# Performance work log

Measured on AMD Instinct MI355X. Metric: run time of the kernel, lower is better.

## Reference

```python
import jax, jax.numpy as jnp
import numpy as np

HEADS = 8
HIDDEN = 1536
HEAD_DIM = HIDDEN // HEADS
SCALE = HEAD_DIM ** -0.5


def setup_inputs() -> dict:
    key = jax.random.key(0)
    ks = jax.random.split(key, 10)
    B, S_IMG, S_TXT = 32, 1024, 77
    w = 0.02
    return {
        "img": jax.random.normal(ks[0], (B, S_IMG, HIDDEN), dtype=jnp.float32),
        "text": jax.random.normal(ks[1], (B, S_TXT, HIDDEN), dtype=jnp.float32),
        "Wq": jax.random.normal(ks[2], (HIDDEN, HIDDEN), dtype=jnp.float32) * w,
        "bq": jnp.zeros((HIDDEN,), dtype=jnp.float32),
        "Wk": jax.random.normal(ks[3], (HIDDEN, HIDDEN), dtype=jnp.float32) * w,
        "bk": jnp.zeros((HIDDEN,), dtype=jnp.float32),
        "Wv": jax.random.normal(ks[4], (HIDDEN, HIDDEN), dtype=jnp.float32) * w,
        "bv": jnp.zeros((HIDDEN,), dtype=jnp.float32),
        "Wo": jax.random.normal(ks[5], (HIDDEN, HIDDEN), dtype=jnp.float32) * w,
        "bo": jnp.zeros((HIDDEN,), dtype=jnp.float32),
    }


def reference(img, text, Wq, bq, Wk, bk, Wv, bv, Wo, bo):
    B, Sq, D = img.shape
    Sk = text.shape[1]
    # QKV projections (nn.Linear: y = x @ W.T + b)
    q = img @ Wq.T + bq    # [B, Sq, D]
    k = text @ Wk.T + bk   # [B, Sk, D]
    v = text @ Wv.T + bv
    # detach trick: position 0 of k/v has gradient stopped; forward value unchanged
    k0 = jax.lax.stop_gradient(k[:, :1, :])
    k = jnp.concatenate([k0, k[:, 1:, :]], axis=1)
    v0 = jax.lax.stop_gradient(v[:, :1, :])
    v = jnp.concatenate([v0, v[:, 1:, :]], axis=1)
    # split heads
    q = q.reshape(B, Sq, HEADS, HEAD_DIM)
    k = k.reshape(B, Sk, HEADS, HEAD_DIM)
    v = v.reshape(B, Sk, HEADS, HEAD_DIM)
    # attention scores and probs (mask is None in this module)
    scores = jnp.einsum("bqhd,bkhd->bhqk", q, k) * SCALE  # [B, H, Sq, Sk]
    probs = jax.nn.softmax(scores, axis=-1)
    out = jnp.einsum("bhqk,bkhd->bqhd", probs, v).reshape(B, Sq, D)
    return out @ Wo.T + bo
```

## Files before the change

kernel.cpp:

```cpp
#include <hip/hip_runtime.h>
#include <hip/hip_bf16.h>


typedef unsigned short u16;
typedef _Float16 f16x8 __attribute__((ext_vector_type(8)));
typedef __attribute__((ext_vector_type(8))) short s16x8;
typedef __attribute__((ext_vector_type(4))) float f32x4;
typedef __attribute__((ext_vector_type(4))) short s16x4;

#define MFMAH(a, b, c) __builtin_amdgcn_mfma_f32_16x16x32_f16(a, b, c, 0, 0, 0)

__device__ __forceinline__ u16 f2h(float x) {
    _Float16 h = (_Float16)x;
    return __builtin_bit_cast(u16, h);
}

__device__ __forceinline__ void gload16(const u16* g, const u16* l) {
    __builtin_amdgcn_global_load_lds(
        (const __attribute__((address_space(1))) unsigned int*)g,
        (__attribute__((address_space(3))) unsigned int*)l, 16, 0, 0);
}

__device__ __forceinline__ int rh(int r) { return (r >> 1) & 3; }

__global__ void conv_h(const float* __restrict__ x, u16* __restrict__ h, int n8) {
    const int i = blockIdx.x * 256 + threadIdx.x;
    if (i >= n8) return;
    const f32x4 a = ((const f32x4*)x)[2 * i];
    const f32x4 b = ((const f32x4*)x)[2 * i + 1];
    u16 o[8];
#pragma unroll
    for (int j = 0; j < 4; ++j) { o[j] = f2h(a[j]); o[4 + j] = f2h(b[j]); }
    *(s16x8*)&h[(size_t)i << 3] = *(s16x8*)o;
}

struct Conv5Args {
    const float* x[5];
    u16* h[5];
    int n8[5];
};

__global__ void conv_h5(Conv5Args A) {
    const int z = blockIdx.y;
    const int i = blockIdx.x * 256 + threadIdx.x;
    if (i >= A.n8[z]) return;
    const float* x = A.x[z];
    const f32x4 a = ((const f32x4*)x)[2 * i];
    const f32x4 b = ((const f32x4*)x)[2 * i + 1];
    u16 o[8];
#pragma unroll
    for (int j = 0; j < 4; ++j) { o[j] = f2h(a[j]); o[4 + j] = f2h(b[j]); }
    *(s16x8*)&A.h[z][(size_t)i << 3] = *(s16x8*)o;
}

template <int OUTF32>
__global__ __launch_bounds__(256, 4) void gemm_h_nt(
    const u16* __restrict__ A,
    const u16* __restrict__ B0, const float* __restrict__ bias0, void* __restrict__ C0,
    const u16* __restrict__ B1, const float* __restrict__ bias1, void* __restrict__ C1,
    int M, int N, int K, int nby) {
    __shared__ u16 lds[16384];

    const u16* B = B0; const float* bias = bias0; void* Cout = C0;
    if (blockIdx.z) { B = B1; bias = bias1; Cout = C1; }

    const int nwg = gridDim.x;
    const int q8 = nwg >> 3, r8 = nwg & 7;
    const int xcd = blockIdx.x & 7, loc = blockIdx.x >> 3;
    const int wgid = (xcd < r8 ? xcd * (q8 + 1) : r8 * (q8 + 1) + (xcd - r8) * q8) + loc;
    const int bx = wgid / nby, by = wgid - bx * nby;
    const int row0 = bx * 128, col0 = by * 128;

    const int t = threadIdx.x, lane = t & 63, w = t >> 6;
    const int wm = w >> 1, wn = w & 1;
    const int l15 = lane & 15, lhi = lane >> 4;

    const u16* gpA[2]; const u16* gpB[2];
    int lofA[2], lofB[2];
#pragma unroll
    for (int it = 0; it < 2; ++it) {
        const int ci = it * 256 + t;
        const int row = ci >> 2, slot = ci & 3;
        const int gs = slot ^ rh(row);
        int ar = row0 + row; if (ar > M - 1) ar = M - 1;
        gpA[it] = A + (size_t)ar * K + (gs << 3);
        gpB[it] = B + (size_t)(col0 + row) * K + (gs << 3);
        lofA[it] = ci * 8;
        lofB[it] = 8192 + ci * 8;
    }

    const int ss = rh(l15);
    int aof[4], bof[4];
#pragma unroll
    for (int i = 0; i < 4; ++i) {
        const int ar = wm * 64 + i * 16 + l15;
        aof[i] = ar * 32 + ((lhi ^ ss) << 3);
        const int br = wn * 64 + i * 16 + l15;
        bof[i] = 8192 + br * 32 + ((lhi ^ ss) << 3);
    }

    f32x4 acc[4][4] = {};
    const int NT = K >> 5;

    for (int tt = 0; tt < NT; ++tt) {
        const size_t kk = (size_t)tt << 5;
        if (tt) __syncthreads();
        gload16(gpA[0] + kk, lds + lofA[0]);
        gload16(gpA[1] + kk, lds + lofA[1]);
        gload16(gpB[0] + kk, lds + lofB[0]);
        gload16(gpB[1] + kk, lds + lofB[1]);
        __syncthreads();

        f16x8 a[4];
#pragma unroll
        for (int mf = 0; mf < 4; ++mf) a[mf] = *(const f16x8*)&lds[aof[mf]];
#pragma unroll
        for (int nf = 0; nf < 4; ++nf) {
            const f16x8 b = *(const f16x8*)&lds[bof[nf]];
#pragma unroll
            for (int mf = 0; mf < 4; ++mf)
                acc[mf][nf] = MFMAH(a[mf], b, acc[mf][nf]);
        }
    }

#pragma unroll
    for (int nf = 0; nf < 4; ++nf) {
        const int col = col0 + wn * 64 + nf * 16 + l15;
        const float bs = bias[col];
#pragma unroll
        for (int mf = 0; mf < 4; ++mf) {
            const int row = row0 + wm * 64 + mf * 16 + (lhi << 2);
#pragma unroll
            for (int r = 0; r < 4; ++r) {
                if (row + r < M) {
                    const float v = acc[mf][nf][r] + bs;
                    if (OUTF32) ((float*)Cout)[(size_t)(row + r) * N + col] = v;
                    else        ((u16*)Cout)[(size_t)(row + r) * N + col] = f2h(v);
                }
            }
        }
    }
}

#define ALDK 200
#define ALDP 104

__global__ void attn_fused(const u16* __restrict__ qbuf, const u16* __restrict__ kbuf,
                           const u16* __restrict__ vbuf, u16* __restrict__ obuf) {
    __shared__ u16 Ks[80 * ALDK];
    __shared__ u16 Pls[64 * ALDP];
    __shared__ u16 Vt[96 * ALDP];

    const int t = threadIdx.x, lane = t & 63, w = t >> 6;
    const int qt = blockIdx.x, h = blockIdx.y, b = blockIdx.z;
    const int l15 = lane & 15, lhi = lane >> 4;

    f16x8 qf[6];
    {
        const size_t qrow = (size_t)(b * 1024 + qt * 64 + w * 16 + l15);
        const u16* qp = qbuf + qrow * 1536 + h * 192 + (lhi << 3);
#pragma unroll
        for (int kt = 0; kt < 6; ++kt) qf[kt] = *(const f16x8*)(qp + kt * 32);
    }

    for (int c = t; c < 80 * 24; c += 256) {
        const int s = c / 24, d8 = (c - s * 24) << 3;
        s16x8 val = {};
        if (s < 77) val = *(const s16x8*)&kbuf[(size_t)(b * 77 + s) * 1536 + h * 192 + d8];
        *(s16x8*)&Ks[s * ALDK + d8] = val;
    }
    for (int c = t; c < 96 * 12; c += 256) {
        const int s = c % 96, d8 = (c / 96) << 3;
        s16x8 val = {};
        if (s < 77) val = *(const s16x8*)&vbuf[(size_t)(b * 77 + s) * 1536 + h * 192 + d8];
#pragma unroll
        for (int j = 0; j < 8; ++j) Vt[(d8 + j) * ALDP + s] = (u16)val[j];
    }
    {
        const int row = w * 16 + l15;
        s16x4 z = {0, 0, 0, 0};
        *(s16x4*)&Pls[row * ALDP + 80 + (lhi << 2)] = z;
    }
    __syncthreads();

    f32x4 sacc[5] = {};
#pragma unroll
    for (int kt = 0; kt < 6; ++kt) {
#pragma unroll
        for (int nf = 0; nf < 5; ++nf) {
            f16x8 kf = *(const f16x8*)&Ks[(nf * 16 + l15) * ALDK + kt * 32 + (lhi << 3)];
            sacc[nf] = MFMAH(qf[kt], kf, sacc[nf]);
        }
    }

    float rps[4];
    const float scale = 0.07216878364870323f;
#pragma unroll
    for (int r = 0; r < 4; ++r) {
        float m = -1e30f;
#pragma unroll
        for (int nf = 0; nf < 5; ++nf) {
            const int c = nf * 16 + l15;
            const float sv = sacc[nf][r] * scale;
            if (c < 77) m = fmaxf(m, sv);
        }
#pragma unroll
        for (int off = 1; off < 16; off <<= 1) m = fmaxf(m, __shfl_xor(m, off));
        float sum = 0.f;
#pragma unroll
        for (int nf = 0; nf < 5; ++nf) {
            const int c = nf * 16 + l15;
            const float p = (c < 77) ? __expf(sacc[nf][r] * scale - m) : 0.f;
            sacc[nf][r] = p;
            sum += p;
        }
#pragma unroll
        for (int off = 1; off < 16; off <<= 1) sum += __shfl_xor(sum, off);
        rps[r] = 1.0f / sum;
    }

#pragma unroll
    for (int r = 0; r < 4; ++r)
#pragma unroll
        for (int nf = 0; nf < 5; ++nf)
            Pls[(w * 16 + (lhi << 2) + r) * ALDP + nf * 16 + l15] = f2h(sacc[nf][r]);
    __syncthreads();

    f16x8 pa[3];
#pragma unroll
    for (int kt = 0; kt < 3; ++kt)
        pa[kt] = *(const f16x8*)&Pls[(w * 16 + l15) * ALDP + kt * 32 + (lhi << 3)];

    const size_t orow = (size_t)(b * 1024 + qt * 64 + w * 16 + (lhi << 2));

    {
        f32x4 oacc[6] = {};
#pragma unroll
        for (int kt = 0; kt < 3; ++kt)
#pragma unroll
            for (int nf = 0; nf < 6; ++nf) {
                f16x8 vf = *(const f16x8*)&Vt[(nf * 16 + l15) * ALDP + kt * 32 + (lhi << 3)];
                oacc[nf] = MFMAH(pa[kt], vf, oacc[nf]);
            }
#pragma unroll
        for (int nf = 0; nf < 6; ++nf) {
            const int col = h * 192 + nf * 16 + l15;
#pragma unroll
            for (int r = 0; r < 4; ++r)
                obuf[(orow + r) * 1536 + col] = f2h(oacc[nf][r] * rps[r]);
        }
    }
    __syncthreads();
    for (int c = t; c < 96 * 12; c += 256) {
        const int s = c % 96, d8 = (c / 96) << 3;
        s16x8 val = {};
        if (s < 77) val = *(const s16x8*)&vbuf[(size_t)(b * 77 + s) * 1536 + h * 192 + 96 + d8];
#pragma unroll
        for (int j = 0; j < 8; ++j) Vt[(d8 + j) * ALDP + s] = (u16)val[j];
    }
    __syncthreads();
    {
        f32x4 oacc[6] = {};
#pragma unroll
        for (int kt = 0; kt < 3; ++kt)
#pragma unroll
            for (int nf = 0; nf < 6; ++nf) {
                f16x8 vf = *(const f16x8*)&Vt[(nf * 16 + l15) * ALDP + kt * 32 + (lhi << 3)];
                oacc[nf] = MFMAH(pa[kt], vf, oacc[nf]);
            }
#pragma unroll
        for (int nf = 0; nf < 6; ++nf) {
            const int col = h * 192 + 96 + nf * 16 + l15;
#pragma unroll
            for (int r = 0; r < 4; ++r)
                obuf[(orow + r) * 1536 + col] = f2h(oacc[nf][r] * rps[r]);
        }
    }
}

extern "C" void kernel_launch(void* const* d_in, const int* in_sizes, int n_in,
                              void* d_out, int out_size, void* d_ws, size_t ws_size,
                              hipStream_t stream) {
    const float* img  = (const float*)d_in[0];
    const float* text = (const float*)d_in[1];
    const float* Wq   = (const float*)d_in[2];
    const float* bq   = (const float*)d_in[3];
    const float* Wk   = (const float*)d_in[4];
    const float* bk   = (const float*)d_in[5];
    const float* Wv   = (const float*)d_in[6];
    const float* bv   = (const float*)d_in[7];
    const float* Wo   = (const float*)d_in[8];
    const float* bo   = (const float*)d_in[9];

    const size_t imgN = (size_t)32768 * 1536;
    const size_t txtN = (size_t)2464 * 1536;
    const size_t wN   = (size_t)1536 * 1536;

    u16* img_h = (u16*)d_ws;
    u16* qb    = img_h + imgN;
    u16* txt_h = qb + imgN;
    u16* Wq_h  = txt_h + txtN;
    u16* Wk_h  = Wq_h + wN;
    u16* Wv_h  = Wk_h + wN;
    u16* Wo_h  = Wv_h + wN;
    u16* kb    = Wo_h + wN;
    u16* vb    = kb + txtN;

    hipLaunchKernelGGL(conv_h, dim3((unsigned)(imgN / 8 / 256)), dim3(256),
                       0, stream, img, img_h, (int)(imgN / 8));
    Conv5Args ca;
    ca.x[0] = text; ca.h[0] = txt_h; ca.n8[0] = (int)(txtN / 8);
    ca.x[1] = Wq;   ca.h[1] = Wq_h;  ca.n8[1] = (int)(wN / 8);
    ca.x[2] = Wk;   ca.h[2] = Wk_h;  ca.n8[2] = (int)(wN / 8);
    ca.x[3] = Wv;   ca.h[3] = Wv_h;  ca.n8[3] = (int)(wN / 8);
    ca.x[4] = Wo;   ca.h[4] = Wo_h;  ca.n8[4] = (int)(wN / 8);
    hipLaunchKernelGGL(conv_h5, dim3((unsigned)((txtN / 8 + 255) / 256), 5),
                       dim3(256), 0, stream, ca);

    hipLaunchKernelGGL((gemm_h_nt<0>), dim3(3072), dim3(256), 0, stream,
                       img_h, Wq_h, bq, (void*)qb, Wq_h, bq, (void*)qb,
                       32768, 1536, 1536, 12);
    hipLaunchKernelGGL((gemm_h_nt<0>), dim3(240, 1, 2), dim3(256), 0, stream,
                       txt_h, Wk_h, bk, (void*)kb, Wv_h, bv, (void*)vb,
                       2464, 1536, 1536, 12);
    hipLaunchKernelGGL(attn_fused, dim3(16, 8, 32), dim3(256), 0, stream,
                       qb, kb, vb, qb);
    hipLaunchKernelGGL((gemm_h_nt<1>), dim3(3072), dim3(256), 0, stream,
                       qb, Wo_h, bo, d_out, Wo_h, bo, d_out,
                       32768, 1536, 1536, 12);
}
```

Measured before the change: 665.4 us.

## Enlarge GEMM tiles to 256x256 and add triple-buffered async LDS pipeline

The fp16 GEMM moves from 128x128 to 256x256 output tiles with an 8x8 MFMA fragment grid per wave. It also replaces the load/sync/compute loop with a three-stage LDS ring, prefetching two K-tiles ahead and waiting on vmcnt before a single barrier per iteration. The goal is to raise arithmetic intensity and hide global-load latency. In exchange, launch bounds drop to one block, register and LDS use grow a lot, and the grid shrinks to 768 blocks, which lowers occupancy. The K/V GEMM, with M=2464, now also pads more rows per tile.

```diff
diff --git a/kernel.cpp b/kernel.cpp
--- a/kernel.cpp
+++ b/kernel.cpp
@@ -54,12 +54,12 @@
 }
 
 template <int OUTF32>
-__global__ __launch_bounds__(256, 4) void gemm_h_nt(
+__global__ __launch_bounds__(256, 1) void gemm_h_nt(
     const u16* __restrict__ A,
     const u16* __restrict__ B0, const float* __restrict__ bias0, void* __restrict__ C0,
     const u16* __restrict__ B1, const float* __restrict__ bias1, void* __restrict__ C1,
     int M, int N, int K, int nby) {
-    __shared__ u16 lds[16384];
+    __shared__ u16 lds[49152];
 
     const u16* B = B0; const float* bias = bias0; void* Cout = C0;
     if (blockIdx.z) { B = B1; bias = bias1; Cout = C1; }
@@ -69,16 +69,16 @@
     const int xcd = blockIdx.x & 7, loc = blockIdx.x >> 3;
     const int wgid = (xcd < r8 ? xcd * (q8 + 1) : r8 * (q8 + 1) + (xcd - r8) * q8) + loc;
     const int bx = wgid / nby, by = wgid - bx * nby;
-    const int row0 = bx * 128, col0 = by * 128;
+    const int row0 = bx * 256, col0 = by * 256;
 
     const int t = threadIdx.x, lane = t & 63, w = t >> 6;
     const int wm = w >> 1, wn = w & 1;
     const int l15 = lane & 15, lhi = lane >> 4;
 
-    const u16* gpA[2]; const u16* gpB[2];
-    int lofA[2], lofB[2];
-#pragma unroll
-    for (int it = 0; it < 2; ++it) {
+    const u16* gpA[4]; const u16* gpB[4];
+    int lofA[4], lofB[4];
+#pragma unroll
+    for (int it = 0; it < 4; ++it) {
         const int ci = it * 256 + t;
         const int row = ci >> 2, slot = ci & 3;
         const int gs = slot ^ rh(row);
@@ -90,46 +90,72 @@
     }
 
     const int ss = rh(l15);
-    int aof[4], bof[4];
-#pragma unroll
-    for (int i = 0; i < 4; ++i) {
-        const int ar = wm * 64 + i * 16 + l15;
+    int aof[8], bof[8];
+#pragma unroll
+    for (int i = 0; i < 8; ++i) {
+        const int ar = wm * 128 + i * 16 + l15;
         aof[i] = ar * 32 + ((lhi ^ ss) << 3);
-        const int br = wn * 64 + i * 16 + l15;
+        const int br = wn * 128 + i * 16 + l15;
         bof[i] = 8192 + br * 32 + ((lhi ^ ss) << 3);
     }
 
-    f32x4 acc[4][4] = {};
+    f32x4 acc[8][8] = {};
     const int NT = K >> 5;
 
+#define SBAR0() __builtin_amdgcn_sched_barrier(0)
+
+#pragma unroll
+    for (int p = 0; p < 2; ++p) {
+        const size_t kp = (size_t)p << 5;
+        u16* lb = lds + (p << 14);
+#pragma unroll
+        for (int it = 0; it < 4; ++it) {
+            gload16(gpA[it] + kp, lb + lofA[it]);
+            gload16(gpB[it] + kp, lb + lofB[it]);
+        }
+    }
+    asm volatile("s_waitcnt vmcnt(8)" ::: "memory");
+    SBAR0(); __builtin_amdgcn_s_barrier(); SBAR0();
+
+    int cur = 0;
     for (int tt = 0; tt < NT; ++tt) {
-        const size_t kk = (size_t)tt << 5;
-        if (tt) __syncthreads();
-        gload16(gpA[0] + kk, lds + lofA[0]);
-        gload16(gpA[1] + kk, lds + lofA[1]);
-        gload16(gpB[0] + kk, lds + lofB[0]);
-        gload16(gpB[1] + kk, lds + lofB[1]);
-        __syncthreads();
-
-        f16x8 a[4];
-#pragma unroll
-        for (int mf = 0; mf < 4; ++mf) a[mf] = *(const f16x8*)&lds[aof[mf]];
-#pragma unroll
-        for (int nf = 0; nf < 4; ++nf) {
-            const f16x8 b = *(const f16x8*)&lds[bof[nf]];
-#pragma unroll
-            for (int mf = 0; mf < 4; ++mf)
-                acc[mf][nf] = MFMAH(a[mf], b, acc[mf][nf]);
-        }
-    }
-
-#pragma unroll
-    for (int nf = 0; nf < 4; ++nf) {
-        const int col = col0 + wn * 64 + nf * 16 + l15;
+        const int cb = cur << 14;
+        int stg = cur + 2; if (stg >= 3) stg -= 3;
+        u16* lsb = lds + (stg << 14);
+        const int tx = (tt + 2 < NT) ? tt + 2 : tt + 2 - NT;
+        const size_t kn = (size_t)tx << 5;
+
+#pragma unroll
+        for (int it = 0; it < 4; ++it) {
+            gload16(gpA[it] + kn, lsb + lofA[it]);
+            gload16(gpB[it] + kn, lsb + lofB[it]);
+        }
+
+        f16x8 a[8];
+#pragma unroll
+        for (int mf = 0; mf < 8; ++mf) a[mf] = *(const f16x8*)&lds[cb + aof[mf]];
+#pragma unroll
+        for (int nf = 0; nf < 8; ++nf) {
+            const f16x8 bfr = *(const f16x8*)&lds[cb + bof[nf]];
+#pragma unroll
+            for (int mf = 0; mf < 8; ++mf)
+                acc[mf][nf] = MFMAH(a[mf], bfr, acc[mf][nf]);
+        }
+
+        asm volatile("s_waitcnt vmcnt(8)" ::: "memory");
+        SBAR0(); __builtin_amdgcn_s_barrier(); SBAR0();
+
+        cur = cur + 1; if (cur == 3) cur = 0;
+    }
+    asm volatile("s_waitcnt vmcnt(0)" ::: "memory");
+
+#pragma unroll
+    for (int nf = 0; nf < 8; ++nf) {
+        const int col = col0 + wn * 128 + nf * 16 + l15;
         const float bs = bias[col];
 #pragma unroll
-        for (int mf = 0; mf < 4; ++mf) {
-            const int row = row0 + wm * 64 + mf * 16 + (lhi << 2);
+        for (int mf = 0; mf < 8; ++mf) {
+            const int row = row0 + wm * 128 + mf * 16 + (lhi << 2);
 #pragma unroll
             for (int r = 0; r < 4; ++r) {
                 if (row + r < M) {
@@ -140,6 +166,7 @@
             }
         }
     }
+#undef SBAR0
 }
 
 #define ALDK 200
@@ -317,15 +344,15 @@
     hipLaunchKernelGGL(conv_h5, dim3((unsigned)((txtN / 8 + 255) / 256), 5),
                        dim3(256), 0, stream, ca);
 
-    hipLaunchKernelGGL((gemm_h_nt<0>), dim3(3072), dim3(256), 0, stream,
+    hipLaunchKernelGGL((gemm_h_nt<0>), dim3(768), dim3(256), 0, stream,
                        img_h, Wq_h, bq, (void*)qb, Wq_h, bq, (void*)qb,
-                       32768, 1536, 1536, 12);
-    hipLaunchKernelGGL((gemm_h_nt<0>), dim3(240, 1, 2), dim3(256), 0, stream,
+                       32768, 1536, 1536, 6);
+    hipLaunchKernelGGL((gemm_h_nt<0>), dim3(60, 1, 2), dim3(256), 0, stream,
                        txt_h, Wk_h, bk, (void*)kb, Wv_h, bv, (void*)vb,
-                       2464, 1536, 1536, 12);
+                       2464, 1536, 1536, 6);
     hipLaunchKernelGGL(attn_fused, dim3(16, 8, 32), dim3(256), 0, stream,
                        qb, kb, vb, qb);
-    hipLaunchKernelGGL((gemm_h_nt<1>), dim3(3072), dim3(256), 0, stream,
+    hipLaunchKernelGGL((gemm_h_nt<1>), dim3(768), dim3(256), 0, stream,
                        qb, Wo_h, bo, d_out, Wo_h, bo, d_out,
-                       32768, 1536, 1536, 12);
-}
+                       32768, 1536, 1536, 6);
+}
```

New measurement: 799.1 us. 20.1% more time.
